# Performance work log

Hardware: AMD Instinct MI355X
Metric: run time of the kernel (lower is better)

The kernel has to match this reference:

```python
import jax, jax.numpy as jnp
import numpy as np

N_NODES = 100000
DEG = 32  # in-degree per node


def setup_inputs() -> dict:
    key = jax.random.key(0)
    ks = jax.random.split(key, 8)
    E = N_NODES * DEG
    x = jax.random.normal(ks[0], (N_NODES, 4), dtype=jnp.float32)
    src = jax.random.randint(ks[1], (E,), 0, N_NODES, dtype=jnp.int32)
    # every node gets exactly DEG incoming messages (DGL mean-reduce semantics)
    dst = jnp.repeat(jnp.arange(N_NODES, dtype=jnp.int32), DEG)
    s = 0.3
    return {
        "x": x, "src": src, "dst": dst,
        "W1": jax.random.normal(ks[2], (4, 32), jnp.float32) * s,
        "b1": jax.random.normal(ks[3], (32,), jnp.float32) * s,
        "W2": jax.random.normal(ks[4], (32, 32), jnp.float32) * s,
        "b2": jax.random.normal(ks[5], (32,), jnp.float32) * s,
        "W3": jax.random.normal(ks[6], (32, 1), jnp.float32) * s,
        "b3": jax.random.normal(ks[7], (1,), jnp.float32) * s,
    }


def _gcn_layer(h, src, dst, deg_inv, W, b):
    # copy_src: gather source features per edge, mean-reduce by destination
    m = jax.ops.segment_sum(h[src], dst, num_segments=N_NODES)
    h_mean = m * deg_inv  # [N, F_in]
    # node apply: ReLU(W h + b)
    return jax.nn.relu(h_mean @ W + b)


def reference(x, src, dst, W1, b1, W2, b2, W3, b3):
    ones = jnp.ones((src.shape[0],), x.dtype)
    deg = jax.ops.segment_sum(ones, dst, num_segments=N_NODES)
    deg_inv = (1.0 / jnp.maximum(deg, 1.0))[:, None]
    h = _gcn_layer(x, src, dst, deg_inv, W1, b1)   # [N, 32]
    h = _gcn_layer(h, src, dst, deg_inv, W2, b2)   # [N, 32]
    h = _gcn_layer(h, src, dst, deg_inv, W3, b3)   # [N, 1]
    return h
```

## Files before the change

kernel.cpp:

```cpp
#include <hip/hip_runtime.h>
#include <hip/hip_bf16.h>

#define N_NODES 100000
#define DEG 32
#define E_TOTAL (3200000LL)

static __device__ __forceinline__ float bf16_lo(unsigned int u) {
    return __uint_as_float(u << 16);
}
static __device__ __forceinline__ float bf16_hi(unsigned int u) {
    return __uint_as_float(u & 0xffff0000u);
}

__global__ __launch_bounds__(256) void gcn_l1(const float* __restrict__ x,
                                              const int* __restrict__ src,
                                              const float* __restrict__ W1,
                                              const float* __restrict__ b1,
                                              __hip_bfloat16* __restrict__ h1) {
    int tid  = blockIdx.x * 256 + threadIdx.x;
    int node = tid >> 5;
    if (node >= N_NODES) return;
    int lane = threadIdx.x & 31;

    int s = src[node * DEG + lane];
    const float4 v = *reinterpret_cast<const float4*>(x + (size_t)s * 4);
    float m0 = v.x, m1 = v.y, m2 = v.z, m3 = v.w;
#pragma unroll
    for (int off = 16; off; off >>= 1) {
        m0 += __shfl_xor(m0, off, 32);
        m1 += __shfl_xor(m1, off, 32);
        m2 += __shfl_xor(m2, off, 32);
        m3 += __shfl_xor(m3, off, 32);
    }
    const float inv = 1.0f / 32.0f;
    m0 *= inv; m1 *= inv; m2 *= inv; m3 *= inv;

    float o = b1[lane];
    o = fmaf(m0, W1[0 * 32 + lane], o);
    o = fmaf(m1, W1[1 * 32 + lane], o);
    o = fmaf(m2, W1[2 * 32 + lane], o);
    o = fmaf(m3, W1[3 * 32 + lane], o);
    h1[(size_t)node * 32 + lane] = __float2bfloat16(fmaxf(o, 0.0f));
}

__global__ __launch_bounds__(256) void gcn_l2(const __hip_bfloat16* __restrict__ h1,
                                              const int* __restrict__ src,
                                              const float* __restrict__ W2,
                                              const float* __restrict__ b2,
                                              const float* __restrict__ W3,
                                              float* __restrict__ g) {
    __shared__ int   sidx[64 * 36];
    __shared__ float mt[64 * 33];
    __shared__ float gpart[4 * 65];

    const int t  = threadIdx.x;
    const long long n0 = (long long)blockIdx.x * 64;

    {
        long long j = n0 * DEG + (long long)t * 8;
        int4 v0, v1;
        if (j + 7 < E_TOTAL) {
            v0 = *reinterpret_cast<const int4*>(src + j);
            v1 = *reinterpret_cast<const int4*>(src + j + 4);
        } else {
            int tmp[8];
#pragma unroll
            for (int m = 0; m < 8; ++m) tmp[m] = (j + m < E_TOTAL) ? src[j + m] : 0;
            v0 = make_int4(tmp[0], tmp[1], tmp[2], tmp[3]);
            v1 = make_int4(tmp[4], tmp[5], tmp[6], tmp[7]);
        }
        int jn = t >> 2;
        int k0 = (t & 3) * 8;
        *reinterpret_cast<int4*>(&sidx[jn * 36 + k0])     = v0;
        *reinterpret_cast<int4*>(&sidx[jn * 36 + k0 + 4]) = v1;
    }
    __syncthreads();

    {
        const int nl = t >> 2;
        const int q  = t & 3;
        const int sb = nl * 36;
        float a0 = 0.f, a1 = 0.f, a2 = 0.f, a3 = 0.f, a4 = 0.f, a5 = 0.f, a6 = 0.f, a7 = 0.f;
        const char* hbase = (const char*)h1 + q * 16;
#pragma unroll
        for (int k = 0; k < 32; ++k) {
            int s = sidx[sb + k];
            const uint4 u = *reinterpret_cast<const uint4*>(hbase + ((size_t)(unsigned)s << 6));
            a0 += bf16_lo(u.x); a1 += bf16_hi(u.x);
            a2 += bf16_lo(u.y); a3 += bf16_hi(u.y);
            a4 += bf16_lo(u.z); a5 += bf16_hi(u.z);
            a6 += bf16_lo(u.w); a7 += bf16_hi(u.w);
        }
        const float inv = 1.0f / 32.0f;
        const int mb = nl * 33 + q * 8;
        mt[mb + 0] = a0 * inv; mt[mb + 1] = a1 * inv;
        mt[mb + 2] = a2 * inv; mt[mb + 3] = a3 * inv;
        mt[mb + 4] = a4 * inv; mt[mb + 5] = a5 * inv;
        mt[mb + 6] = a6 * inv; mt[mb + 7] = a7 * inv;
    }
    __syncthreads();

    {
        const int w = __builtin_amdgcn_readfirstlane(t >> 6);
        const int l = t & 63;
        const float* __restrict__ b2w = b2 + w * 8;
        const float* __restrict__ w3w = W3 + w * 8;
        float o[8];
#pragma unroll
        for (int j = 0; j < 8; ++j) o[j] = b2w[j];
        const int rb = l * 33;
#pragma unroll
        for (int k = 0; k < 32; ++k) {
            const float mk = mt[rb + k];
            const float* __restrict__ w2r = W2 + k * 32 + w * 8;
#pragma unroll
            for (int j = 0; j < 8; ++j) o[j] = fmaf(mk, w2r[j], o[j]);
        }
        float p = 0.f;
#pragma unroll
        for (int j = 0; j < 8; ++j) p += fmaxf(o[j], 0.f) * w3w[j];
        gpart[w * 65 + l] = p;
    }
    __syncthreads();

    if (t < 64) {
        float s = gpart[t] + gpart[65 + t] + gpart[130 + t] + gpart[195 + t];
        long long node = n0 + t;
        if (node < N_NODES) g[node] = s;
    }
}

__global__ __launch_bounds__(256) void gcn_l3(const float* __restrict__ g,
                                              const int* __restrict__ src,
                                              const float* __restrict__ b3,
                                              float* __restrict__ out) {
    int tid  = blockIdx.x * 256 + threadIdx.x;
    int node = tid >> 5;
    if (node >= N_NODES) return;
    int lane = threadIdx.x & 31;

    float p = g[src[node * DEG + lane]];
#pragma unroll
    for (int off = 16; off; off >>= 1) p += __shfl_xor(p, off, 32);
    if (lane == 0) out[node] = fmaxf(p * (1.0f / 32.0f) + b3[0], 0.0f);
}

extern "C" void kernel_launch(void* const* d_in, const int* in_sizes, int n_in,
                              void* d_out, int out_size, void* d_ws, size_t ws_size,
                              hipStream_t stream) {
    const float* x   = (const float*)d_in[0];
    const int*   src = (const int*)d_in[1];
    const float* W1  = (const float*)d_in[3];
    const float* b1  = (const float*)d_in[4];
    const float* W2  = (const float*)d_in[5];
    const float* b2  = (const float*)d_in[6];
    const float* W3  = (const float*)d_in[7];
    const float* b3  = (const float*)d_in[8];
    float* out = (float*)d_out;

    __hip_bfloat16* h1 = (__hip_bfloat16*)d_ws;
    float* g = (float*)((char*)d_ws + (size_t)N_NODES * 32 * sizeof(__hip_bfloat16));

    dim3 block(256);
    gcn_l1<<<dim3((N_NODES * DEG + 255) / 256), block, 0, stream>>>(x, src, W1, b1, h1);
    gcn_l2<<<dim3((N_NODES + 63) / 64),        block, 0, stream>>>(h1, src, W2, b2, W3, g);
    gcn_l3<<<dim3((N_NODES * DEG + 255) / 256), block, 0, stream>>>(g, src, b3, out);
}
```

Baseline: 142.6 us.

## Restructure layer 1 and 3 kernels to 64 nodes per block with staged indices

Layers 1 and 3 move from one-lane-per-edge with wave shuffle reductions to the 64-nodes-per-block scheme already used by layer 2. Each block stages the edge indices into shared memory with vectorized loads, and each thread gathers 8 neighbours before a shared-memory partial reduction. Layer 1 also writes eight packed bf16 values per thread with a 16-byte store and a manual round-to-nearest-even conversion. This is meant to cut the number of launched threads, the shuffle traffic and the narrow stores, in exchange for extra barriers and shared memory.

```diff
diff --git a/kernel.cpp b/kernel.cpp
--- a/kernel.cpp
+++ b/kernel.cpp
@@ -10,6 +10,31 @@
 }
 static __device__ __forceinline__ float bf16_hi(unsigned int u) {
     return __uint_as_float(u & 0xffff0000u);
+}
+static __device__ __forceinline__ unsigned short f2bf_rne(float f) {
+    unsigned int u = __float_as_uint(f);
+    u += 0x7fffu + ((u >> 16) & 1u);
+    return (unsigned short)(u >> 16);
+}
+
+static __device__ __forceinline__ void stage_idx(const int* __restrict__ src,
+                                                 long long n0, int t, int* sidx) {
+    long long j = n0 * DEG + (long long)t * 8;
+    int4 v0, v1;
+    if (j + 7 < E_TOTAL) {
+        v0 = *reinterpret_cast<const int4*>(src + j);
+        v1 = *reinterpret_cast<const int4*>(src + j + 4);
+    } else {
+        int tmp[8];
+#pragma unroll
+        for (int m = 0; m < 8; ++m) tmp[m] = (j + m < E_TOTAL) ? src[j + m] : 0;
+        v0 = make_int4(tmp[0], tmp[1], tmp[2], tmp[3]);
+        v1 = make_int4(tmp[4], tmp[5], tmp[6], tmp[7]);
+    }
+    int jn = t >> 2;
+    int k0 = (t & 3) * 8;
+    *reinterpret_cast<int4*>(&sidx[jn * 36 + k0])     = v0;
+    *reinterpret_cast<int4*>(&sidx[jn * 36 + k0 + 4]) = v1;
 }
 
 __global__ __launch_bounds__(256) void gcn_l1(const float* __restrict__ x,
@@ -17,30 +42,68 @@
                                               const float* __restrict__ W1,
                                               const float* __restrict__ b1,
                                               __hip_bfloat16* __restrict__ h1) {
-    int tid  = blockIdx.x * 256 + threadIdx.x;
-    int node = tid >> 5;
-    if (node >= N_NODES) return;
-    int lane = threadIdx.x & 31;
-
-    int s = src[node * DEG + lane];
-    const float4 v = *reinterpret_cast<const float4*>(x + (size_t)s * 4);
-    float m0 = v.x, m1 = v.y, m2 = v.z, m3 = v.w;
-#pragma unroll
-    for (int off = 16; off; off >>= 1) {
-        m0 += __shfl_xor(m0, off, 32);
-        m1 += __shfl_xor(m1, off, 32);
-        m2 += __shfl_xor(m2, off, 32);
-        m3 += __shfl_xor(m3, off, 32);
-    }
-    const float inv = 1.0f / 32.0f;
-    m0 *= inv; m1 *= inv; m2 *= inv; m3 *= inv;
-
-    float o = b1[lane];
-    o = fmaf(m0, W1[0 * 32 + lane], o);
-    o = fmaf(m1, W1[1 * 32 + lane], o);
-    o = fmaf(m2, W1[2 * 32 + lane], o);
-    o = fmaf(m3, W1[3 * 32 + lane], o);
-    h1[(size_t)node * 32 + lane] = __float2bfloat16(fmaxf(o, 0.0f));
+    __shared__ int    sidx[64 * 36];
+    __shared__ float4 pm4[64 * 5];
+
+    const int t = threadIdx.x;
+    const long long n0 = (long long)blockIdx.x * 64;
+
+    stage_idx(src, n0, t, sidx);
+    __syncthreads();
+
+    const int nl = t >> 2;
+    const int q  = t & 3;
+    {
+        const int4 i0 = *reinterpret_cast<const int4*>(&sidx[nl * 36 + q * 8]);
+        const int4 i1 = *reinterpret_cast<const int4*>(&sidx[nl * 36 + q * 8 + 4]);
+        const int idx[8] = { i0.x, i0.y, i0.z, i0.w, i1.x, i1.y, i1.z, i1.w };
+        float a0 = 0.f, a1 = 0.f, a2 = 0.f, a3 = 0.f;
+#pragma unroll
+        for (int m = 0; m < 8; ++m) {
+            const float4 v = *reinterpret_cast<const float4*>(x + ((size_t)(unsigned)idx[m] << 2));
+            a0 += v.x; a1 += v.y; a2 += v.z; a3 += v.w;
+        }
+        pm4[nl * 5 + q] = make_float4(a0, a1, a2, a3);
+    }
+    __syncthreads();
+
+    {
+        const float4 p0 = pm4[nl * 5 + 0];
+        const float4 p1 = pm4[nl * 5 + 1];
+        const float4 p2 = pm4[nl * 5 + 2];
+        const float4 p3 = pm4[nl * 5 + 3];
+        const float inv = 1.0f / 32.0f;
+        const float m0 = (p0.x + p1.x + p2.x + p3.x) * inv;
+        const float m1 = (p0.y + p1.y + p2.y + p3.y) * inv;
+        const float m2 = (p0.z + p1.z + p2.z + p3.z) * inv;
+        const float m3 = (p0.w + p1.w + p2.w + p3.w) * inv;
+
+        const int f0 = q * 8;
+        float o[8];
+#pragma unroll
+        for (int j = 0; j < 8; ++j) o[j] = b1[f0 + j];
+        const float* w0 = W1 + 0 * 32 + f0;
+        const float* w1 = W1 + 1 * 32 + f0;
+        const float* w2 = W1 + 2 * 32 + f0;
+        const float* w3 = W1 + 3 * 32 + f0;
+#pragma unroll
+        for (int j = 0; j < 8; ++j) {
+            float oj = o[j];
+            oj = fmaf(m0, w0[j], oj);
+            oj = fmaf(m1, w1[j], oj);
+            oj = fmaf(m2, w2[j], oj);
+            oj = fmaf(m3, w3[j], oj);
+            o[j] = oj;
+        }
+
+        const long long node = n0 + nl;
+        if (node < N_NODES) {
+            union { unsigned short us[8]; uint4 v; } pk;
+#pragma unroll
+            for (int j = 0; j < 8; ++j) pk.us[j] = f2bf_rne(fmaxf(o[j], 0.0f));
+            *reinterpret_cast<uint4*>((char*)h1 + ((size_t)node << 6) + (size_t)f0 * 2) = pk.v;
+        }
+    }
 }
 
 __global__ __launch_bounds__(256) void gcn_l2(const __hip_bfloat16* __restrict__ h1,
@@ -56,24 +119,7 @@
     const int t  = threadIdx.x;
     const long long n0 = (long long)blockIdx.x * 64;
 
-    {
-        long long j = n0 * DEG + (long long)t * 8;
-        int4 v0, v1;
-        if (j + 7 < E_TOTAL) {
-            v0 = *reinterpret_cast<const int4*>(src + j);
-            v1 = *reinterpret_cast<const int4*>(src + j + 4);
-        } else {
-            int tmp[8];
-#pragma unroll
-            for (int m = 0; m < 8; ++m) tmp[m] = (j + m < E_TOTAL) ? src[j + m] : 0;
-            v0 = make_int4(tmp[0], tmp[1], tmp[2], tmp[3]);
-            v1 = make_int4(tmp[4], tmp[5], tmp[6], tmp[7]);
-        }
-        int jn = t >> 2;
-        int k0 = (t & 3) * 8;
-        *reinterpret_cast<int4*>(&sidx[jn * 36 + k0])     = v0;
-        *reinterpret_cast<int4*>(&sidx[jn * 36 + k0 + 4]) = v1;
-    }
+    stage_idx(src, n0, t, sidx);
     __syncthreads();
 
     {
@@ -134,15 +180,35 @@
                                               const int* __restrict__ src,
                                               const float* __restrict__ b3,
                                               float* __restrict__ out) {
-    int tid  = blockIdx.x * 256 + threadIdx.x;
-    int node = tid >> 5;
-    if (node >= N_NODES) return;
-    int lane = threadIdx.x & 31;
-
-    float p = g[src[node * DEG + lane]];
-#pragma unroll
-    for (int off = 16; off; off >>= 1) p += __shfl_xor(p, off, 32);
-    if (lane == 0) out[node] = fmaxf(p * (1.0f / 32.0f) + b3[0], 0.0f);
+    __shared__ int   sidx[64 * 36];
+    __shared__ float ps[64 * 5];
+
+    const int t = threadIdx.x;
+    const long long n0 = (long long)blockIdx.x * 64;
+
+    stage_idx(src, n0, t, sidx);
+    __syncthreads();
+
+    {
+        const int nl = t >> 2;
+        const int q  = t & 3;
+        const int4 i0 = *reinterpret_cast<const int4*>(&sidx[nl * 36 + q * 8]);
+        const int4 i1 = *reinterpret_cast<const int4*>(&sidx[nl * 36 + q * 8 + 4]);
+        const int idx[8] = { i0.x, i0.y, i0.z, i0.w, i1.x, i1.y, i1.z, i1.w };
+        float s = 0.f;
+#pragma unroll
+        for (int m = 0; m < 8; ++m) s += g[(unsigned)idx[m]];
+        ps[nl * 5 + q] = s;
+    }
+    __syncthreads();
+
+    if (t < 64) {
+        const long long node = n0 + t;
+        if (node < N_NODES) {
+            float s = ps[t * 5 + 0] + ps[t * 5 + 1] + ps[t * 5 + 2] + ps[t * 5 + 3];
+            out[node] = fmaxf(s * (1.0f / 32.0f) + b3[0], 0.0f);
+        }
+    }
 }
 
 extern "C" void kernel_launch(void* const* d_in, const int* in_sizes, int n_in,
@@ -162,7 +228,8 @@
     float* g = (float*)((char*)d_ws + (size_t)N_NODES * 32 * sizeof(__hip_bfloat16));
 
     dim3 block(256);
-    gcn_l1<<<dim3((N_NODES * DEG + 255) / 256), block, 0, stream>>>(x, src, W1, b1, h1);
-    gcn_l2<<<dim3((N_NODES + 63) / 64),        block, 0, stream>>>(h1, src, W2, b2, W3, g);
-    gcn_l3<<<dim3((N_NODES * DEG + 255) / 256), block, 0, stream>>>(g, src, b3, out);
-}
+    dim3 grid((N_NODES + 63) / 64);
+    gcn_l1<<<grid, block, 0, stream>>>(x, src, W1, b1, h1);
+    gcn_l2<<<grid, block, 0, stream>>>(h1, src, W2, b2, W3, g);
+    gcn_l3<<<grid, block, 0, stream>>>(g, src, b3, out);
+}
```

Result: no change. 141.9 us (-0.5%).
